# Kernel tuning notes

Hardware: AMD Instinct MI355X
Metric: run time of the kernel (lower is better)

## Reference

```python
import jax, jax.numpy as jnp
import numpy as np

WIN = 8     # sliding-chunk window size (Long2DSCSelfAttention default w=8)
HEADS = 8   # num_heads


def setup_inputs() -> dict:
    key = jax.random.key(0)
    ks = jax.random.split(key, 3)
    B, C, H, W = 4, 512, 64, 64
    x = jax.random.normal(ks[0], (B, C, H, W), jnp.float32)
    w_qkv = jax.random.normal(ks[1], (3 * C, C), jnp.float32) * 0.02
    b_qkv = jnp.zeros((3 * C,), jnp.float32)
    w_proj = jax.random.normal(ks[2], (C, C), jnp.float32) * 0.02
    b_proj = jnp.zeros((C,), jnp.float32)
    return {"x": x, "w_qkv": w_qkv, "b_qkv": b_qkv, "w_proj": w_proj, "b_proj": b_proj}


def _chunk(t, nh, nw, win):
    B, _, _, h, d = t.shape
    t = t.reshape(B, nh, win, nw, win, h, d)
    return t.transpose(0, 5, 1, 3, 2, 4, 6).reshape(B, h, nh, nw, win * win, d)


def reference(x, w_qkv, b_qkv, w_proj, b_proj):
    B, C, H, W = x.shape
    win, heads = WIN, HEADS
    d = C // heads
    nh, nw = H // win, W // win
    m = win * win  # tokens per chunk

    xf = x.transpose(0, 2, 3, 1)                      # [B,H,W,C]
    qkv = xf @ w_qkv.T + b_qkv                        # [B,H,W,3C]
    qkv = qkv.reshape(B, H, W, 3, heads, d)
    q = _chunk(qkv[..., 0, :, :], nh, nw, win)        # [B,h,nh,nw,m,d]
    k = _chunk(qkv[..., 1, :, :], nh, nw, win)
    v = _chunk(qkv[..., 2, :, :], nh, nw, win)

    # pad chunk grid by one chunk on each side; gather 3x3 chunk neighborhoods
    kp = jnp.pad(k, ((0, 0), (0, 0), (1, 1), (1, 1), (0, 0), (0, 0)))
    vp = jnp.pad(v, ((0, 0), (0, 0), (1, 1), (1, 1), (0, 0), (0, 0)))
    k9 = jnp.concatenate([kp[:, :, i:i + nh, j:j + nw] for i in range(3) for j in range(3)], axis=4)  # [B,h,nh,nw,9m,d]
    v9 = jnp.concatenate([vp[:, :, i:i + nh, j:j + nw] for i in range(3) for j in range(3)], axis=4)

    # validity mask for neighbor chunks at the image boundary
    valid = jnp.pad(jnp.ones((nh, nw), bool), ((1, 1), (1, 1)))
    vmask = jnp.concatenate(
        [jnp.repeat(valid[i:i + nh, j:j + nw][..., None], m, axis=-1) for i in range(3) for j in range(3)],
        axis=-1)                                      # [nh,nw,9m]

    scale = float(d) ** -0.5
    attn = jnp.einsum('bhxyqd,bhxykd->bhxyqk', q * scale, k9)      # [B,h,nh,nw,m,9m]
    neg = jnp.asarray(-1e9, attn.dtype)
    attn = jnp.where(vmask[None, None, :, :, None, :], attn, neg)
    attn = jax.nn.softmax(attn, axis=-1)
    out = jnp.einsum('bhxyqk,bhxykd->bhxyqd', attn, v9)            # [B,h,nh,nw,m,d]

    out = out.reshape(B, heads, nh, nw, win, win, d)
    out = out.transpose(0, 2, 4, 3, 5, 1, 6).reshape(B, H, W, C)
    out = out @ w_proj.T + b_proj
    return out.transpose(0, 3, 1, 2)                               # [B,C,H,W]
```

## Files before the change

### kernel.cpp

```cpp
#include <hip/hip_runtime.h>
#include <cstdint>
#include <cstddef>

namespace {

constexpr int kC = 512;
constexpr int kHW = 4096;
constexpr int kHeads = 8;
constexpr int kChunkElems = 64 * 64;

typedef float f32x4 __attribute__((ext_vector_type(4)));
typedef _Float16 f16x8 __attribute__((ext_vector_type(8)));
union FragU { uint4 u; f16x8 h; };

__device__ __forceinline__ ushort f16rn(float x) {
  _Float16 h = (_Float16)x;
  ushort u;
  __builtin_memcpy(&u, &h, 2);
  return u;
}
__device__ __forceinline__ uint pack2(ushort a, ushort b) {
  return (uint)a | ((uint)b << 16);
}
__device__ __forceinline__ float fexp2(float x) {
  return exp2f(x);
}
__device__ __forceinline__ uint pkrtz(float a, float b) {
  auto h = __builtin_amdgcn_cvt_pkrtz(a, b);
  uint u;
  __builtin_memcpy(&u, &h, 4);
  return u;
}
__device__ __forceinline__ void gld16(const void* g, void* lds) {
  __builtin_amdgcn_global_load_lds(
      (const __attribute__((address_space(1))) uint32_t*)g,
      (__attribute__((address_space(3))) uint32_t*)lds, 16, 0, 0);
}

__global__ __launch_bounds__(256)
void convw16_kernel(const float* __restrict__ w, ushort* __restrict__ wh)
{
  int idx = (blockIdx.x * 256 + threadIdx.x) * 8;
  float4 v0 = *(const float4*)(w + idx);
  float4 v1 = *(const float4*)(w + idx + 4);
  float xs[8] = {v0.x, v0.y, v0.z, v0.w, v1.x, v1.y, v1.z, v1.w};
  ushort hh[8];
#pragma unroll
  for (int e = 0; e < 8; ++e) hh[e] = f16rn(xs[e]);
  *(uint4*)(wh + idx) = make_uint4(pack2(hh[0], hh[1]), pack2(hh[2], hh[3]),
                                   pack2(hh[4], hh[5]), pack2(hh[6], hh[7]));
}

__global__ __launch_bounds__(256)
void convx_kernel(const float* __restrict__ x, ushort* __restrict__ xt)
{
  __shared__ float LT[64][68];
  const int tid = threadIdx.x;
  const int t0 = blockIdx.x * 64;
  const int c0 = blockIdx.y * 64;
  const int b  = blockIdx.z;
  const float* xb = x + (size_t)b * kC * kHW;

#pragma unroll
  for (int u = 0; u < 4; ++u) {
    int idx = tid + u * 256;
    int rc = idx >> 4;
    int t4 = (idx & 15) << 2;
    float4 val = *(const float4*)(xb + (size_t)(c0 + rc) * kHW + t0 + t4);
    LT[t4 + 0][rc] = val.x;
    LT[t4 + 1][rc] = val.y;
    LT[t4 + 2][rc] = val.z;
    LT[t4 + 3][rc] = val.w;
  }
  __syncthreads();
#pragma unroll
  for (int u = 0; u < 4; ++u) {
    int idx = tid + u * 256;
    int rt = idx >> 4;
    int c4 = (idx & 15) << 2;
    float4 v = *(const float4*)&LT[rt][c4];
    size_t o = ((size_t)b * kHW + t0 + rt) * kC + c0 + c4;
    *(ushort4*)(xt + o) = make_ushort4(f16rn(v.x), f16rn(v.y),
                                       f16rn(v.z), f16rn(v.w));
  }
}

__global__ __launch_bounds__(256)
void qkv_mfma_kernel(const ushort* __restrict__ xt,
                     const ushort* __restrict__ wq,
                     const float* __restrict__ bqkv,
                     ushort* __restrict__ qo, ushort* __restrict__ ko,
                     ushort* __restrict__ vo)
{
  __shared__ __align__(16) ushort As[128 * 64];
  __shared__ __align__(16) ushort Bs[128 * 64];

  const int tid  = threadIdx.x;
  const int lane = tid & 63;
  const int wv   = tid >> 6;
  const int quad = lane >> 4;
  const int l15  = lane & 15;
  const int wm = wv & 1, wn = wv >> 1;
  const int m0 = blockIdx.x * 128;
  const int n0 = blockIdx.y * 128;
  const int b  = blockIdx.z;

  const ushort* xb = xt + (size_t)b * kHW * kC;

  f32x4 acc[4][4];
#pragma unroll
  for (int i = 0; i < 4; ++i)
#pragma unroll
    for (int j = 0; j < 4; ++j) acc[i][j] = (f32x4){0.f, 0.f, 0.f, 0.f};

  for (int k0 = 0; k0 < kC; k0 += 64) {
    __syncthreads();
#pragma unroll
    for (int ii = 0; ii < 4; ++ii) {
      int i = wv * 4 + ii;
      int m = i * 8 + (lane >> 3);
      int gch = (lane & 7) ^ (m & 7);
      size_t goA = (size_t)(m0 + m) * kC + k0 + gch * 8;
      gld16(xb + goA, (char*)As + i * 1024);
      size_t goB = (size_t)(n0 + m) * kC + k0 + gch * 8;
      gld16(wq + goB, (char*)Bs + i * 1024);
    }
    __syncthreads();

#pragma unroll
    for (int s = 0; s < 2; ++s) {
      const int gq = s * 4 + quad;
      FragU aA[4], bB[4];
#pragma unroll
      for (int mi = 0; mi < 4; ++mi) {
        int mr = wm * 64 + mi * 16 + l15;
        int off = mr * 64 + ((gq ^ (mr & 7)) * 8);
        aA[mi].u = *(const uint4*)&As[off];
      }
#pragma unroll
      for (int ni = 0; ni < 4; ++ni) {
        int nr = wn * 64 + ni * 16 + l15;
        int off = nr * 64 + ((gq ^ (nr & 7)) * 8);
        bB[ni].u = *(const uint4*)&Bs[off];
      }
#pragma unroll
      for (int mi = 0; mi < 4; ++mi)
#pragma unroll
        for (int ni = 0; ni < 4; ++ni)
          acc[mi][ni] = __builtin_amdgcn_mfma_f32_16x16x32_f16(aA[mi].h, bB[ni].h, acc[mi][ni], 0, 0, 0);
    }
  }

  const int sec = n0 >> 9;
  const int jwbase = n0 + wn * 64;
  const int head = (jwbase >> 6) & 7;
  const size_t hbb = ((size_t)b * kHeads + head) * 64;
  float biasv[4];
#pragma unroll
  for (int ni = 0; ni < 4; ++ni) biasv[ni] = bqkv[jwbase + ni * 16 + l15];

  if (sec == 2) {
#pragma unroll
    for (int ni = 0; ni < 4; ++ni) {
      int dd = ni * 16 + l15;
#pragma unroll
      for (int mi = 0; mi < 4; ++mi) {
        int t0t = m0 + wm * 64 + mi * 16 + quad * 4;
        int h = t0t >> 6, w = t0t & 63;
        int cy = h >> 3, iy = h & 7, cx = w >> 3, ix = w & 7;
        size_t cb = (hbb + cy * 8 + cx) * (size_t)kChunkElems;
        int tokb = iy * 8 + ix;
        ushort hh[4];
#pragma unroll
        for (int r = 0; r < 4; ++r) hh[r] = f16rn(acc[mi][ni][r] + biasv[ni]);
        *(ushort4*)(vo + cb + (size_t)dd * 64 + tokb) = make_ushort4(hh[0], hh[1], hh[2], hh[3]);
      }
    }
  } else {
    __syncthreads();
    ushort* dst = (sec == 0) ? qo : ko;
    const float sc = (sec == 0) ? 0.125f * 1.44269504089f : 1.0f;
    ushort* tH = As + wv * 1152;
    const int ltok = lane >> 2;
    const int dd0 = (lane & 3) * 16;
#pragma unroll
    for (int mi = 0; mi < 4; ++mi) {
#pragma unroll
      for (int ni = 0; ni < 4; ++ni)
#pragma unroll
        for (int r = 0; r < 4; ++r)
          tH[(quad * 4 + r) * 68 + ni * 16 + l15] =
              f16rn((acc[mi][ni][r] + biasv[ni]) * sc);
      int tg = m0 + wm * 64 + mi * 16 + ltok;
      int h = tg >> 6, w = tg & 63;
      int cy = h >> 3, iy = h & 7, cx = w >> 3, ix = w & 7;
      size_t cb = (hbb + cy * 8 + cx) * (size_t)kChunkElems
                + (size_t)(iy * 8 + ix) * 64 + dd0;
      uint4 h0 = *(const uint4*)&tH[ltok * 68 + dd0];
      uint4 h1 = *(const uint4*)&tH[ltok * 68 + dd0 + 8];
      *(uint4*)(dst + cb) = h0;
      *(uint4*)(dst + cb + 8) = h1;
    }
  }
}

__global__ __launch_bounds__(256)
void attn_mfma_kernel(const ushort* __restrict__ qg, const ushort* __restrict__ kg,
                      const ushort* __restrict__ vg,
                      ushort* __restrict__ ao)
{
  __shared__ __align__(16) ushort KB[4096], VB[4096];
  __shared__ __align__(16) ushort Ps[4 * 16 * 72];

  const int tid  = threadIdx.x;
  const int lane = tid & 63;
  const int wv   = tid >> 6;
  const int quad = lane >> 4;
  const int l15  = lane & 15;

  const int bx = blockIdx.x;
  const int g  = (bx & 7) * 4 + ((bx >> 3) >> 6);
  const int c  = (bx >> 3) & 63;
  const int b = g >> 3, head = g & 7;
  const int cy = c >> 3, cx = c & 7;

  const size_t hb = (size_t)b * kHeads + head;
  const size_t gbase = hb * 64 * (size_t)kChunkElems;
  const size_t cbase = gbase + (size_t)c * (size_t)kChunkElems;

  FragU aQ0, aQ1;
  {
    const ushort* qr = qg + cbase + (size_t)(wv * 16 + l15) * 64 + quad * 8;
    aQ0.u = *(const uint4*)(qr);
    aQ1.u = *(const uint4*)(qr + 32);
  }

  const int boff = ((lane >> 3) * 64) + (((lane & 7) ^ (lane >> 3)) * 8);
  const ushort* kgB = kg + gbase + boff + (size_t)(wv * 2) * 512;
  const ushort* vgB = vg + gbase + boff + (size_t)(wv * 2) * 512;
  char* kDst0 = (char*)KB + (wv * 2) * 1024;
  char* vDst0 = (char*)VB + (wv * 2) * 1024;

  int kvOff0[4], kvOff1[4];
  {
    const int sw = l15 & 7;
#pragma unroll
    for (int nt = 0; nt < 4; ++nt) {
      int row = nt * 16 + l15;
      kvOff0[nt] = row * 64 + ((quad ^ sw) * 8);
      kvOff1[nt] = row * 64 + (((4 + quad) ^ sw) * 8);
    }
  }

  ushort* PsW = Ps + wv * 1152;
  ushort* pWr = PsW + l15 * 72 + quad * 4;
  const ushort* pRd = PsW + l15 * 72 + quad * 8;

  unsigned long long list = 0ull;
  int cnt = 0;
#pragma unroll
  for (int p = 0; p < 9; ++p) {
    const int dy = p / 3 - 1, dx = p % 3 - 1;
    int ny = cy + dy, nx = cx + dx;
    if ((unsigned)ny < 8u && (unsigned)nx < 8u) {
      list |= (unsigned long long)(ny * 8 + nx) << (6 * cnt);
      ++cnt;
    }
  }

  f32x4 o[4];
#pragma unroll
  for (int r = 0; r < 4; ++r) o[r] = (f32x4){0.f, 0.f, 0.f, 0.f};
  float rsum = 0.f;

  {
    int ch0 = (int)(list & 63);
    const ushort* pk = kgB + (size_t)ch0 * kChunkElems;
    gld16(pk, kDst0);
    gld16(pk + 512, kDst0 + 1024);
    const ushort* pv = vgB + (size_t)ch0 * kChunkElems;
    gld16(pv, vDst0);
    gld16(pv + 512, vDst0 + 1024);
  }

  for (int i = 0; i < cnt; ++i) {
    const bool more = (i + 1 < cnt);
    const int chn = (int)((list >> (6 * (i + 1))) & 63);

    asm volatile("s_waitcnt vmcnt(2)" ::: "memory");
    asm volatile("s_barrier" ::: "memory");

    FragU kf[8];
#pragma unroll
    for (int nt = 0; nt < 4; ++nt) {
      kf[nt * 2].u     = *(const uint4*)&KB[kvOff0[nt]];
      kf[nt * 2 + 1].u = *(const uint4*)&KB[kvOff1[nt]];
    }
    asm volatile("s_waitcnt lgkmcnt(0)" ::: "memory");
    asm volatile("s_waitcnt vmcnt(0)" ::: "memory");
    asm volatile("s_barrier" ::: "memory");

    if (more) {
      const ushort* pk = kgB + (size_t)chn * kChunkElems;
      gld16(pk, kDst0);
      gld16(pk + 512, kDst0 + 1024);
    }

    f32x4 s[4];
#pragma unroll
    for (int nt = 0; nt < 4; ++nt) s[nt] = (f32x4){0.f, 0.f, 0.f, 0.f};
#pragma unroll
    for (int nt = 0; nt < 4; ++nt) {
      s[nt] = __builtin_amdgcn_mfma_f32_16x16x32_f16(kf[nt * 2].h, aQ0.h, s[nt], 0, 0, 0);
      s[nt] = __builtin_amdgcn_mfma_f32_16x16x32_f16(kf[nt * 2 + 1].h, aQ1.h, s[nt], 0, 0, 0);
    }

#pragma unroll
    for (int nt = 0; nt < 4; ++nt) {
      float e0 = fexp2(s[nt][0]);
      float e1 = fexp2(s[nt][1]);
      float e2 = fexp2(s[nt][2]);
      float e3 = fexp2(s[nt][3]);
      rsum += (e0 + e1) + (e2 + e3);
      *(uint2*)(pWr + nt * 16) = make_uint2(pkrtz(e0, e1), pkrtz(e2, e3));
    }

    FragU aP0, aP1;
    aP0.u = *(const uint4*)(pRd);
    aP1.u = *(const uint4*)(pRd + 32);

#pragma unroll
    for (int nt = 0; nt < 4; ++nt) {
      FragU v0, v1;
      v0.u = *(const uint4*)&VB[kvOff0[nt]];
      v1.u = *(const uint4*)&VB[kvOff1[nt]];
      o[nt] = __builtin_amdgcn_mfma_f32_16x16x32_f16(v0.h, aP0.h, o[nt], 0, 0, 0);
      o[nt] = __builtin_amdgcn_mfma_f32_16x16x32_f16(v1.h, aP1.h, o[nt], 0, 0, 0);
    }

    asm volatile("s_waitcnt lgkmcnt(0)" ::: "memory");
    asm volatile("s_barrier" ::: "memory");
    if (more) {
      const ushort* pv = vgB + (size_t)chn * kChunkElems;
      gld16(pv, vDst0);
      gld16(pv + 512, vDst0 + 1024);
    }
  }

  rsum += __shfl_xor(rsum, 16, 64);
  rsum += __shfl_xor(rsum, 32, 64);
  const float inv = 1.0f / rsum;

  const int trg = wv * 16 + l15;
  const int hp = cy * 8 + (trg >> 3);
  const int wp = cx * 8 + (trg & 7);
  const size_t obase = ((size_t)b * kHW + hp * 64 + wp) * (size_t)kC + head * 64;

#pragma unroll
  for (int nt = 0; nt < 4; ++nt) {
    float v0 = o[nt][0] * inv;
    float v1 = o[nt][1] * inv;
    float v2 = o[nt][2] * inv;
    float v3 = o[nt][3] * inv;
    *(ushort4*)(ao + obase + nt * 16 + quad * 4) =
        make_ushort4(f16rn(v0), f16rn(v1), f16rn(v2), f16rn(v3));
  }
}

__global__ __launch_bounds__(256)
void proj_mfma_kernel(const ushort* __restrict__ ao,
                      const ushort* __restrict__ wp,
                      const float* __restrict__ bproj,
                      float* __restrict__ out)
{
  __shared__ __align__(16) ushort As[128 * 64];
  __shared__ __align__(16) ushort Bs[64 * 64];

  const int tid  = threadIdx.x;
  const int lane = tid & 63;
  const int wv   = tid >> 6;
  const int quad = lane >> 4;
  const int l15  = lane & 15;
  const int wm = wv & 1, wn = wv >> 1;
  const int n0g = blockIdx.x * 64;
  const int m0  = blockIdx.y * 128;
  const int b   = n0g >> 12;
  const int tl0 = n0g & 4095;

  f32x4 acc[4][2];
#pragma unroll
  for (int i = 0; i < 4; ++i)
#pragma unroll
    for (int j = 0; j < 2; ++j) acc[i][j] = (f32x4){0.f, 0.f, 0.f, 0.f};

  for (int k0 = 0; k0 < kC; k0 += 64) {
    __syncthreads();
#pragma unroll
    for (int ii = 0; ii < 4; ++ii) {
      int i = wv * 4 + ii;
      int m = i * 8 + (lane >> 3);
      int gch = (lane & 7) ^ (m & 7);
      size_t goA = (size_t)(m0 + m) * kC + k0 + gch * 8;
      gld16(wp + goA, (char*)As + i * 1024);
    }
#pragma unroll
    for (int ii = 0; ii < 2; ++ii) {
      int i = wv * 2 + ii;
      int m = i * 8 + (lane >> 3);
      int gch = (lane & 7) ^ (m & 7);
      size_t goB = (size_t)(n0g + m) * kC + k0 + gch * 8;
      gld16(ao + goB, (char*)Bs + i * 1024);
    }
    __syncthreads();

#pragma unroll
    for (int s = 0; s < 2; ++s) {
      const int gq = s * 4 + quad;
      FragU aA[4], bB[2];
#pragma unroll
      for (int mi = 0; mi < 4; ++mi) {
        int mr = wm * 64 + mi * 16 + l15;
        int off = mr * 64 + ((gq ^ (mr & 7)) * 8);
        aA[mi].u = *(const uint4*)&As[off];
      }
#pragma unroll
      for (int ni = 0; ni < 2; ++ni) {
        int nr = wn * 32 + ni * 16 + l15;
        int off = nr * 64 + ((gq ^ (nr & 7)) * 8);
        bB[ni].u = *(const uint4*)&Bs[off];
      }
#pragma unroll
      for (int mi = 0; mi < 4; ++mi)
#pragma unroll
        for (int ni = 0; ni < 2; ++ni)
          acc[mi][ni] = __builtin_amdgcn_mfma_f32_16x16x32_f16(aA[mi].h, bB[ni].h, acc[mi][ni], 0, 0, 0);
    }
  }

#pragma unroll
  for (int mi = 0; mi < 4; ++mi)
#pragma unroll
    for (int r = 0; r < 4; ++r) {
      int c = m0 + wm * 64 + mi * 16 + quad * 4 + r;
      float bias = bproj[c];
      size_t rowb = ((size_t)b * kC + c) * (size_t)kHW + tl0 + wn * 32;
#pragma unroll
      for (int ni = 0; ni < 2; ++ni)
        out[rowb + ni * 16 + l15] = acc[mi][ni][r] + bias;
    }
}

}

extern "C" void kernel_launch(void* const* d_in, const int* in_sizes, int n_in,
                              void* d_out, int out_size, void* d_ws, size_t ws_size,
                              hipStream_t stream)
{
  const float* x     = (const float*)d_in[0];
  const float* wqkv  = (const float*)d_in[1];
  const float* bqkv  = (const float*)d_in[2];
  const float* wproj = (const float*)d_in[3];
  const float* bproj = (const float*)d_in[4];
  float* out = (float*)d_out;

  const size_t seg = (size_t)2048 * kChunkElems;
  ushort* base = (ushort*)d_ws;
  ushort* qb = base + 0 * seg;
  ushort* kb = base + 1 * seg;
  ushort* vb = base + 2 * seg;
  ushort* xt = base + 3 * seg;
  ushort* ao = xt;
  ushort* wqh = base + 5 * seg;
  ushort* wp16 = qb;

  convw16_kernel<<<dim3(384), 256, 0, stream>>>(wqkv, wqh);
  convx_kernel<<<dim3(64, 8, 4), 256, 0, stream>>>(x, xt);
  qkv_mfma_kernel<<<dim3(32, 12, 4), 256, 0, stream>>>(xt, wqh, bqkv,
                                                       qb, kb, vb);
  attn_mfma_kernel<<<dim3(2048), 256, 0, stream>>>(qb, kb, vb, ao);
  convw16_kernel<<<dim3(128), 256, 0, stream>>>(wproj, wp16);
  proj_mfma_kernel<<<dim3(256, 4), 256, 0, stream>>>(ao, wp16, bproj, out);
}
```

Baseline: 187.7 us.

## Double-buffer LDS tiles in QKV and projection GEMM kernels

Both MFMA GEMM kernels now keep two LDS buffers and issue the global-to-LDS loads for the next k-tile before computing on the current one. A single waitcnt and barrier per iteration replaces the two syncthreads, so global load latency can overlap with MFMA work. LDS use per block doubles (64KB for QKV), which may lower occupancy. The hand-written waitcnt/barrier sequence has to stay correct for the async buffer_load-to-LDS path.

```diff
diff --git a/kernel.cpp b/kernel.cpp
--- a/kernel.cpp
+++ b/kernel.cpp
@@ -92,8 +92,8 @@
                      ushort* __restrict__ qo, ushort* __restrict__ ko,
                      ushort* __restrict__ vo)
 {
-  __shared__ __align__(16) ushort As[128 * 64];
-  __shared__ __align__(16) ushort Bs[128 * 64];
+  __shared__ __align__(16) ushort As[2][128 * 64];
+  __shared__ __align__(16) ushort Bs[2][128 * 64];
 
   const int tid  = threadIdx.x;
   const int lane = tid & 63;
@@ -107,26 +107,35 @@
 
   const ushort* xb = xt + (size_t)b * kHW * kC;
 
-  f32x4 acc[4][4];
-#pragma unroll
-  for (int i = 0; i < 4; ++i)
-#pragma unroll
-    for (int j = 0; j < 4; ++j) acc[i][j] = (f32x4){0.f, 0.f, 0.f, 0.f};
-
-  for (int k0 = 0; k0 < kC; k0 += 64) {
-    __syncthreads();
+  auto stage = [&](int buf, int k0) {
 #pragma unroll
     for (int ii = 0; ii < 4; ++ii) {
       int i = wv * 4 + ii;
       int m = i * 8 + (lane >> 3);
       int gch = (lane & 7) ^ (m & 7);
       size_t goA = (size_t)(m0 + m) * kC + k0 + gch * 8;
-      gld16(xb + goA, (char*)As + i * 1024);
+      gld16(xb + goA, (char*)&As[buf][0] + i * 1024);
       size_t goB = (size_t)(n0 + m) * kC + k0 + gch * 8;
-      gld16(wq + goB, (char*)Bs + i * 1024);
-    }
-    __syncthreads();
-
+      gld16(wq + goB, (char*)&Bs[buf][0] + i * 1024);
+    }
+  };
+
+  f32x4 acc[4][4];
+#pragma unroll
+  for (int i = 0; i < 4; ++i)
+#pragma unroll
+    for (int j = 0; j < 4; ++j) acc[i][j] = (f32x4){0.f, 0.f, 0.f, 0.f};
+
+  stage(0, 0);
+  asm volatile("s_waitcnt vmcnt(0)" ::: "memory");
+  asm volatile("s_barrier" ::: "memory");
+
+  for (int kt = 0; kt < 8; ++kt) {
+    const int cur = kt & 1;
+    if (kt < 7) stage(cur ^ 1, (kt + 1) * 64);
+
+    const ushort* Ac = &As[cur][0];
+    const ushort* Bc = &Bs[cur][0];
 #pragma unroll
     for (int s = 0; s < 2; ++s) {
       const int gq = s * 4 + quad;
@@ -135,13 +144,13 @@
       for (int mi = 0; mi < 4; ++mi) {
         int mr = wm * 64 + mi * 16 + l15;
         int off = mr * 64 + ((gq ^ (mr & 7)) * 8);
-        aA[mi].u = *(const uint4*)&As[off];
+        aA[mi].u = *(const uint4*)&Ac[off];
       }
 #pragma unroll
       for (int ni = 0; ni < 4; ++ni) {
         int nr = wn * 64 + ni * 16 + l15;
         int off = nr * 64 + ((gq ^ (nr & 7)) * 8);
-        bB[ni].u = *(const uint4*)&Bs[off];
+        bB[ni].u = *(const uint4*)&Bc[off];
       }
 #pragma unroll
       for (int mi = 0; mi < 4; ++mi)
@@ -149,6 +158,10 @@
         for (int ni = 0; ni < 4; ++ni)
           acc[mi][ni] = __builtin_amdgcn_mfma_f32_16x16x32_f16(aA[mi].h, bB[ni].h, acc[mi][ni], 0, 0, 0);
     }
+
+    asm volatile("s_waitcnt lgkmcnt(0)" ::: "memory");
+    if (kt < 7) asm volatile("s_waitcnt vmcnt(0)" ::: "memory");
+    asm volatile("s_barrier" ::: "memory");
   }
 
   const int sec = n0 >> 9;
@@ -177,10 +190,9 @@
       }
     }
   } else {
-    __syncthreads();
     ushort* dst = (sec == 0) ? qo : ko;
     const float sc = (sec == 0) ? 0.125f * 1.44269504089f : 1.0f;
-    ushort* tH = As + wv * 1152;
+    ushort* tH = &As[0][0] + wv * 1152;
     const int ltok = lane >> 2;
     const int dd0 = (lane & 3) * 16;
 #pragma unroll
@@ -373,8 +385,8 @@
                       const float* __restrict__ bproj,
                       float* __restrict__ out)
 {
-  __shared__ __align__(16) ushort As[128 * 64];
-  __shared__ __align__(16) ushort Bs[64 * 64];
+  __shared__ __align__(16) ushort As[2][128 * 64];
+  __shared__ __align__(16) ushort Bs[2][64 * 64];
 
   const int tid  = threadIdx.x;
   const int lane = tid & 63;
@@ -387,21 +399,14 @@
   const int b   = n0g >> 12;
   const int tl0 = n0g & 4095;
 
-  f32x4 acc[4][2];
-#pragma unroll
-  for (int i = 0; i < 4; ++i)
-#pragma unroll
-    for (int j = 0; j < 2; ++j) acc[i][j] = (f32x4){0.f, 0.f, 0.f, 0.f};
-
-  for (int k0 = 0; k0 < kC; k0 += 64) {
-    __syncthreads();
+  auto stage = [&](int buf, int k0) {
 #pragma unroll
     for (int ii = 0; ii < 4; ++ii) {
       int i = wv * 4 + ii;
       int m = i * 8 + (lane >> 3);
       int gch = (lane & 7) ^ (m & 7);
       size_t goA = (size_t)(m0 + m) * kC + k0 + gch * 8;
-      gld16(wp + goA, (char*)As + i * 1024);
+      gld16(wp + goA, (char*)&As[buf][0] + i * 1024);
     }
 #pragma unroll
     for (int ii = 0; ii < 2; ++ii) {
@@ -409,10 +414,26 @@
       int m = i * 8 + (lane >> 3);
       int gch = (lane & 7) ^ (m & 7);
       size_t goB = (size_t)(n0g + m) * kC + k0 + gch * 8;
-      gld16(ao + goB, (char*)Bs + i * 1024);
-    }
-    __syncthreads();
-
+      gld16(ao + goB, (char*)&Bs[buf][0] + i * 1024);
+    }
+  };
+
+  f32x4 acc[4][2];
+#pragma unroll
+  for (int i = 0; i < 4; ++i)
+#pragma unroll
+    for (int j = 0; j < 2; ++j) acc[i][j] = (f32x4){0.f, 0.f, 0.f, 0.f};
+
+  stage(0, 0);
+  asm volatile("s_waitcnt vmcnt(0)" ::: "memory");
+  asm volatile("s_barrier" ::: "memory");
+
+  for (int kt = 0; kt < 8; ++kt) {
+    const int cur = kt & 1;
+    if (kt < 7) stage(cur ^ 1, (kt + 1) * 64);
+
+    const ushort* Ac = &As[cur][0];
+    const ushort* Bc = &Bs[cur][0];
 #pragma unroll
     for (int s = 0; s < 2; ++s) {
       const int gq = s * 4 + quad;
@@ -421,13 +442,13 @@
       for (int mi = 0; mi < 4; ++mi) {
         int mr = wm * 64 + mi * 16 + l15;
         int off = mr * 64 + ((gq ^ (mr & 7)) * 8);
-        aA[mi].u = *(const uint4*)&As[off];
+        aA[mi].u = *(const uint4*)&Ac[off];
       }
 #pragma unroll
       for (int ni = 0; ni < 2; ++ni) {
         int nr = wn * 32 + ni * 16 + l15;
         int off = nr * 64 + ((gq ^ (nr & 7)) * 8);
-        bB[ni].u = *(const uint4*)&Bs[off];
+        bB[ni].u = *(const uint4*)&Bc[off];
       }
 #pragma unroll
       for (int mi = 0; mi < 4; ++mi)
@@ -435,6 +456,10 @@
         for (int ni = 0; ni < 2; ++ni)
           acc[mi][ni] = __builtin_amdgcn_mfma_f32_16x16x32_f16(aA[mi].h, bB[ni].h, acc[mi][ni], 0, 0, 0);
     }
+
+    asm volatile("s_waitcnt lgkmcnt(0)" ::: "memory");
+    if (kt < 7) asm volatile("s_waitcnt vmcnt(0)" ::: "memory");
+    asm volatile("s_barrier" ::: "memory");
   }
 
 #pragma unroll
```

Result: slower. 192.3 us (+2.5%).
